# Kernel tuning notes

Hardware: AMD Instinct MI355X
Metric: run time of the kernel (lower is better)

The kernel has to match this reference:

```python
import jax, jax.numpy as jnp
import numpy as np
from jax import lax

B, L, D, DM, S, M, P = 8, 2048, 512, 1024, 32, 4, 4096


def setup_inputs() -> dict:
    key = jax.random.key(0)
    ks = jax.random.split(key, 13)
    emb = jax.random.normal(ks[0], (B, L, D), jnp.float32)
    pos = jax.random.randint(ks[1], (B, L), 1, P + 1)          # pos >= 1 (0 reserved for CLS)
    sid = jax.random.randint(ks[2], (B, L), 0, S)
    mod = jax.random.randint(ks[3], (B, L), 0, M)
    role = jax.random.randint(ks[4], (B, L), 0, 3)
    padding_mask = jax.random.uniform(ks[5], (B, L)) < 0.9
    W_proj = jax.random.normal(ks[6], (S, DM, D), jnp.float32) / np.float32(np.sqrt(D))
    b_proj = jax.random.normal(ks[7], (S, DM), jnp.float32) * 0.01
    cls_content = jax.random.normal(ks[8], (DM,), jnp.float32)
    pos_emb = jax.random.normal(ks[9], (P + 1, DM), jnp.float32) * 0.02
    id_emb = jax.random.normal(ks[10], (S + 1, DM), jnp.float32) * 0.02
    mod_emb = jax.random.normal(ks[11], (M, DM), jnp.float32) * 0.02
    role_emb = jax.random.normal(ks[12], (3, DM), jnp.float32) * 0.02
    return dict(emb=emb, pos=pos, sid=sid, mod=mod, role=role, padding_mask=padding_mask,
                W_proj=W_proj, b_proj=b_proj, cls_content=cls_content,
                pos_emb=pos_emb, id_emb=id_emb, mod_emb=mod_emb, role_emb=role_emb)


def _moe_project(emb, sid, padding_mask, W_proj, b_proj):
    """Per-token per-signal Linear: tokens[b,l] = W_proj[sid[b,l]] @ emb[b,l] + b_proj[sid[b,l]].
    Computed as S dense GEMMs masked per token (dense-dispatch MoE), avoiding an
    O(B*L*DM*D) gathered-weight tensor."""
    def step(acc, sWb):
        s, W, b = sWb
        y = jnp.einsum('bld,od->blo', emb, W) + b  # (B, L, DM)
        m = (sid == s) & padding_mask              # padded tokens stay zero
        return acc + jnp.where(m[..., None], y, 0.0), None
    acc0 = jnp.zeros(emb.shape[:2] + (W_proj.shape[1],), emb.dtype)
    acc, _ = lax.scan(step, acc0, (jnp.arange(W_proj.shape[0]), W_proj, b_proj))
    return acc


def reference(emb, pos, sid, mod, role, padding_mask,
              W_proj, b_proj, cls_content, pos_emb, id_emb, mod_emb, role_emb):
    Bc, Lc = pos.shape
    dm = cls_content.shape[0]
    cls_id = id_emb.shape[0] - 1  # == num_signals

    proj = _moe_project(emb, sid, padding_mask, W_proj, b_proj)  # (B, L, DM)

    cls = jnp.broadcast_to(cls_content, (Bc, 1, dm))
    tokens = jnp.concatenate([cls, proj], axis=1)                # (B, L+1, DM)

    pos_full = jnp.concatenate([jnp.zeros((Bc, 1), pos.dtype), pos], axis=1)
    sid_full = jnp.concatenate([jnp.full((Bc, 1), cls_id, sid.dtype), sid], axis=1)
    tokens = tokens + pos_emb[pos_full] + id_emb[sid_full]

    # modality + role embeddings only on non-CLS tokens (added even where padded, as in torch)
    tokens = tokens.at[:, 1:, :].add(mod_emb[mod] + role_emb[role])

    attn_keep = jnp.concatenate([jnp.ones((Bc, 1), bool), padding_mask], axis=1)
    return tokens, attn_keep
```

## Files before the change

kernel.cpp:

```cpp
#include <hip/hip_runtime.h>
#include <hip/hip_bf16.h>


#define NB   8
#define NL   2048
#define ND   512
#define NDM  1024
#define NS   32
#define NTOK (NB * NL)
#define LP1  (NL + 1)
#define MAXTILES 160
#define EXP_CAP 1024

static __device__ __forceinline__ size_t attn_off() { return (size_t)NB * LP1 * NDM; }

typedef __attribute__((ext_vector_type(8))) short bf16x8;
typedef __attribute__((ext_vector_type(4))) float f32x4;

__device__ __forceinline__ unsigned short f2bf(float f) {
    unsigned int x = __float_as_uint(f);
    x += 0x7fffu + ((x >> 16) & 1u);
    return (unsigned short)(x >> 16);
}

__device__ __forceinline__ float bf2f(unsigned short s) {
    return __uint_as_float(((unsigned int)s) << 16);
}

__device__ __forceinline__ bf16x8 cvt8(float4 a, float4 b) {
    bf16x8 r;
    r[0] = (short)__bfloat16_as_ushort(__float2bfloat16(a.x));
    r[1] = (short)__bfloat16_as_ushort(__float2bfloat16(a.y));
    r[2] = (short)__bfloat16_as_ushort(__float2bfloat16(a.z));
    r[3] = (short)__bfloat16_as_ushort(__float2bfloat16(a.w));
    r[4] = (short)__bfloat16_as_ushort(__float2bfloat16(b.x));
    r[5] = (short)__bfloat16_as_ushort(__float2bfloat16(b.y));
    r[6] = (short)__bfloat16_as_ushort(__float2bfloat16(b.z));
    r[7] = (short)__bfloat16_as_ushort(__float2bfloat16(b.w));
    return r;
}

__device__ __forceinline__ float4 ld4(const float* p) { return *(const float4*)p; }
__device__ __forceinline__ float4 add4(float4 a, float4 b) {
    return make_float4(a.x + b.x, a.y + b.y, a.z + b.z, a.w + b.w);
}

__global__ void k_bucket(const int* __restrict__ sid, const int* __restrict__ mask,
                         const int* __restrict__ mod, const int* __restrict__ role,
                         const float* __restrict__ me, const float* __restrict__ re,
                         int* __restrict__ cnt, int* __restrict__ kidx,
                         int* __restrict__ tokList, float* __restrict__ mrT,
                         float* __restrict__ out) {
    int t = blockIdx.x * 256 + threadIdx.x;
    if (t < NTOK) {
        int s = sid[t];
        bool keep = mask[t] != 0;
        int b = t >> 11, l = t & (NL - 1);
        out[attn_off() + (size_t)b * LP1 + l + 1] = keep ? 1.0f : 0.0f;
        if (t < NB) out[attn_off() + (size_t)t * LP1] = 1.0f;
        int ki = -1;
        if (keep) {
            ki = atomicAdd(&cnt[s], 1);
            if (ki < EXP_CAP) tokList[s * EXP_CAP + ki] = t;
        }
        kidx[t] = ki;
    }
    if (blockIdx.x < 12) {
        int mr = blockIdx.x, m = mr / 3, ro = mr % 3;
        int o = threadIdx.x * 4;
        float4 v = add4(ld4(me + (size_t)m * NDM + o), ld4(re + (size_t)ro * NDM + o));
        *(float4*)&mrT[(size_t)mr * NDM + o] = v;
    }
}

__global__ __launch_bounds__(256) void k_gemm(
    const float* __restrict__ emb, const float* __restrict__ Wp,
    const int* __restrict__ tokList, const int* __restrict__ cnt,
    unsigned short* __restrict__ projC) {
    int e = -1, rowBase = 0, nRows = 0, cBase = 0;
    {
        int T = blockIdx.y, idx = 0, cb = 0;
        for (int s = 0; s < NS; ++s) {
            int c = min(cnt[s], EXP_CAP);
            int nt = (c + 127) >> 7;
            if (T >= idx && T < idx + nt) {
                e = s; rowBase = (T - idx) * 128;
                nRows = min(128, c - rowBase); cBase = cb + rowBase;
            }
            idx += nt; cb += c;
        }
        if (e < 0) return;
    }
    const int nBase = blockIdx.x * 128;

    __shared__ short SA[2][128 * 32];
    __shared__ short SB[2][128 * 32];

    const int tid  = threadIdx.x;
    const int lane = tid & 63;
    const int w    = tid >> 6;
    const int wr   = w >> 1, wc = w & 1;
    const int fr   = lane & 15, kg = lane >> 4;

    const int srow = tid >> 2;
    const int sch  = tid & 3;
    const size_t eBase = (size_t)e * EXP_CAP + rowBase;
    int ar0 = (srow < nRows) ? srow : 0;
    int ar1 = (srow + 64 < nRows) ? srow + 64 : 0;
    int tok0 = tokList[eBase + ar0];
    int tok1 = tokList[eBase + ar1];
    const float* a0 = emb + (size_t)tok0 * ND + sch * 8;
    const float* a1 = emb + (size_t)tok1 * ND + sch * 8;
    const float* b0 = Wp + ((size_t)e * NDM + nBase + srow) * ND + sch * 8;
    const float* b1 = Wp + ((size_t)e * NDM + nBase + srow + 64) * ND + sch * 8;
    const int wo0 = srow * 32 + (sch ^ ((srow >> 1) & 3)) * 8;
    const int wo1 = wo0 + 64 * 32;

    f32x4 acc[4][4];
#pragma unroll
    for (int i = 0; i < 4; ++i)
#pragma unroll
        for (int j = 0; j < 4; ++j)
            acc[i][j] = (f32x4){0.f, 0.f, 0.f, 0.f};

    float4 ta0a, ta0b, ta1a, ta1b, tb0a, tb0b, tb1a, tb1b;
    bf16x8 na0, na1, nb0, nb1;

#define LDF(ks) do {                                           \
        ta0a = ld4(a0 + (ks) * 32); ta0b = ld4(a0 + (ks) * 32 + 4); \
        ta1a = ld4(a1 + (ks) * 32); ta1b = ld4(a1 + (ks) * 32 + 4); \
        tb0a = ld4(b0 + (ks) * 32); tb0b = ld4(b0 + (ks) * 32 + 4); \
        tb1a = ld4(b1 + (ks) * 32); tb1b = ld4(b1 + (ks) * 32 + 4); \
    } while (0)
#define CVT() do {                                             \
        na0 = cvt8(ta0a, ta0b); na1 = cvt8(ta1a, ta1b);        \
        nb0 = cvt8(tb0a, tb0b); nb1 = cvt8(tb1a, tb1b);        \
    } while (0)

    LDF(0); CVT();
    *(bf16x8*)&SA[0][wo0] = na0;
    *(bf16x8*)&SA[0][wo1] = na1;
    *(bf16x8*)&SB[0][wo0] = nb0;
    *(bf16x8*)&SB[0][wo1] = nb1;
    LDF(1); CVT();

    const int pc = kg ^ ((fr >> 1) & 3);
    for (int ks = 0; ks < ND / 32; ++ks) {
        const int cur = ks & 1;
        __syncthreads();
        if (ks < ND / 32 - 1) {
            *(bf16x8*)&SA[cur ^ 1][wo0] = na0;
            *(bf16x8*)&SA[cur ^ 1][wo1] = na1;
            *(bf16x8*)&SB[cur ^ 1][wo0] = nb0;
            *(bf16x8*)&SB[cur ^ 1][wo1] = nb1;
        }
        if (ks < ND / 32 - 2) LDF(ks + 2);
        bf16x8 af[4], bv[4];
#pragma unroll
        for (int i = 0; i < 4; ++i)
            af[i] = *(const bf16x8*)&SA[cur][(wr * 64 + i * 16 + fr) * 32 + pc * 8];
#pragma unroll
        for (int j = 0; j < 4; ++j)
            bv[j] = *(const bf16x8*)&SB[cur][(wc * 64 + j * 16 + fr) * 32 + pc * 8];
#pragma unroll
        for (int i = 0; i < 4; ++i)
#pragma unroll
            for (int j = 0; j < 4; ++j)
                acc[i][j] = __builtin_amdgcn_mfma_f32_16x16x32_bf16(af[i], bv[j], acc[i][j], 0, 0, 0);
        if (ks < ND / 32 - 2) CVT();
    }
#undef LDF
#undef CVT

#pragma unroll
    for (int i = 0; i < 4; ++i) {
#pragma unroll
        for (int r = 0; r < 4; ++r) {
            int row = wr * 64 + i * 16 + kg * 4 + r;
            if (row < nRows) {
                size_t crow = (size_t)(cBase + row) * NDM + nBase;
#pragma unroll
                for (int j = 0; j < 4; ++j)
                    projC[crow + wc * 64 + j * 16 + fr] = f2bf(acc[i][j][r]);
            }
        }
    }
}

__global__ void k_out(const int* __restrict__ pos, const int* __restrict__ sid,
                      const int* __restrict__ mod, const int* __restrict__ role,
                      const int* __restrict__ mask, const int* __restrict__ kidx,
                      const int* __restrict__ cnt,
                      const float* __restrict__ bp, const float* __restrict__ cls_c,
                      const float* __restrict__ pe, const float* __restrict__ ie,
                      const float* __restrict__ mrT,
                      const unsigned short* __restrict__ projC,
                      float* __restrict__ out) {
    __shared__ int scnt[NS];
    if (threadIdx.x < NS) scnt[threadIdx.x] = min(cnt[threadIdx.x], EXP_CAP);
    __syncthreads();
    int rp = threadIdx.x >> 7;
    int o  = (threadIdx.x & 127) * 8;
    int l1 = blockIdx.x * 2 + rp;
    int b  = blockIdx.y;
    if (l1 > NL) return;
    float4 v0, v1;
    if (l1 == 0) {
        const float* ieC = ie + (size_t)NS * NDM;
        v0 = add4(add4(ld4(cls_c + o), ld4(pe + o)), ld4(ieC + o));
        v1 = add4(add4(ld4(cls_c + o + 4), ld4(pe + o + 4)), ld4(ieC + o + 4));
    } else {
        int t = b * NL + l1 - 1;
        int p = pos[t], s = sid[t], mr = mod[t] * 3 + role[t];
        const float* peR = pe + (size_t)p * NDM + o;
        const float* ieR = ie + (size_t)s * NDM + o;
        const float* mrR = mrT + (size_t)mr * NDM + o;
        v0 = add4(add4(ld4(peR), ld4(ieR)), ld4(mrR));
        v1 = add4(add4(ld4(peR + 4), ld4(ieR + 4)), ld4(mrR + 4));
        if (mask[t] != 0) {
            const float* bpR = bp + (size_t)s * NDM + o;
            v0 = add4(v0, ld4(bpR));
            v1 = add4(v1, ld4(bpR + 4));
            int ki = kidx[t];
            if (ki >= 0 && ki < EXP_CAP) {
                int boff = 0;
                for (int q = 0; q < s; ++q) boff += scnt[q];
                const unsigned short* pr = projC + (size_t)(boff + ki) * NDM + o;
                v0.x += bf2f(pr[0]); v0.y += bf2f(pr[1]);
                v0.z += bf2f(pr[2]); v0.w += bf2f(pr[3]);
                v1.x += bf2f(pr[4]); v1.y += bf2f(pr[5]);
                v1.z += bf2f(pr[6]); v1.w += bf2f(pr[7]);
            }
        }
    }
    float* dst = &out[((size_t)b * LP1 + l1) * NDM + o];
    *(float4*)dst = v0;
    *(float4*)(dst + 4) = v1;
}

extern "C" void kernel_launch(void* const* d_in, const int* in_sizes, int n_in,
                              void* d_out, int out_size, void* d_ws, size_t ws_size,
                              hipStream_t stream) {
    const float* emb  = (const float*)d_in[0];
    const int* pos    = (const int*)d_in[1];
    const int* sid    = (const int*)d_in[2];
    const int* mod    = (const int*)d_in[3];
    const int* role   = (const int*)d_in[4];
    const int* mask   = (const int*)d_in[5];
    const float* Wp   = (const float*)d_in[6];
    const float* bp   = (const float*)d_in[7];
    const float* cls  = (const float*)d_in[8];
    const float* pe   = (const float*)d_in[9];
    const float* ie   = (const float*)d_in[10];
    const float* me   = (const float*)d_in[11];
    const float* re   = (const float*)d_in[12];
    float* out = (float*)d_out;

    int* ws        = (int*)d_ws;
    int* cnt       = ws;
    int* tokList   = ws + 1024;
    int* kidx      = ws + 33792;
    float* mrT     = (float*)(ws + 50176);
    unsigned short* projC = (unsigned short*)((char*)d_ws + 262144);

    hipMemsetAsync(cnt, 0, 32 * sizeof(int), stream);
    k_bucket<<<NTOK / 256, 256, 0, stream>>>(sid, mask, mod, role, me, re,
                                             cnt, kidx, tokList, mrT, out);

    dim3 gg(NDM / 128, MAXTILES);
    k_gemm<<<gg, 256, 0, stream>>>(emb, Wp, tokList, cnt, projC);

    dim3 go((LP1 + 1) / 2, NB);
    k_out<<<go, 256, 0, stream>>>(pos, sid, mod, role, mask, kidx, cnt,
                                  bp, cls, pe, ie, mrT, projC, out);
}
```

Measured before the change: 122.6 us.

## Widen GEMM tile to 128x256 with 512 threads to reuse A loads

The grouped-expert GEMM tile grows from 128x128 to 128x256 output columns and the block from 256 to 512 threads (8 waves in a 2x4 grid). Each gathered emb row is now loaded and converted once per 256 output columns instead of once per 128, which halves redundant A traffic and conversion work. The cost is half as many blocks per tile row, so there is less parallelism on a grid that is already sparse in active tiles, along with more shared memory per block and a new launch-bounds occupancy hint.

```diff
diff --git a/kernel.cpp b/kernel.cpp
--- a/kernel.cpp
+++ b/kernel.cpp
@@ -73,7 +73,7 @@
     }
 }
 
-__global__ __launch_bounds__(256) void k_gemm(
+__global__ __launch_bounds__(512, 4) void k_gemm(
     const float* __restrict__ emb, const float* __restrict__ Wp,
     const int* __restrict__ tokList, const int* __restrict__ cnt,
     unsigned short* __restrict__ projC) {
@@ -91,30 +91,30 @@
         }
         if (e < 0) return;
     }
-    const int nBase = blockIdx.x * 128;
+    const int nBase = blockIdx.x * 256;
 
     __shared__ short SA[2][128 * 32];
-    __shared__ short SB[2][128 * 32];
+    __shared__ short SB[2][256 * 32];
 
     const int tid  = threadIdx.x;
     const int lane = tid & 63;
     const int w    = tid >> 6;
-    const int wr   = w >> 1, wc = w & 1;
+    const int wr   = w >> 2, wc = w & 3;
     const int fr   = lane & 15, kg = lane >> 4;
 
-    const int srow = tid >> 2;
-    const int sch  = tid & 3;
+    const int srowA = tid >> 2;
+    const int schA  = tid & 3;
     const size_t eBase = (size_t)e * EXP_CAP + rowBase;
-    int ar0 = (srow < nRows) ? srow : 0;
-    int ar1 = (srow + 64 < nRows) ? srow + 64 : 0;
-    int tok0 = tokList[eBase + ar0];
-    int tok1 = tokList[eBase + ar1];
-    const float* a0 = emb + (size_t)tok0 * ND + sch * 8;
-    const float* a1 = emb + (size_t)tok1 * ND + sch * 8;
-    const float* b0 = Wp + ((size_t)e * NDM + nBase + srow) * ND + sch * 8;
-    const float* b1 = Wp + ((size_t)e * NDM + nBase + srow + 64) * ND + sch * 8;
-    const int wo0 = srow * 32 + (sch ^ ((srow >> 1) & 3)) * 8;
-    const int wo1 = wo0 + 64 * 32;
+    int arA = (srowA < nRows) ? srowA : 0;
+    int tokA = tokList[eBase + arA];
+    const float* aP = emb + (size_t)tokA * ND + schA * 8;
+    const int woA = srowA * 32 + (schA ^ ((srowA >> 1) & 3)) * 8;
+
+    const int srowB = tid >> 1;
+    const int halfB = tid & 1;
+    const float* bP = Wp + ((size_t)e * NDM + nBase + srowB) * ND + halfB * 16;
+    const int woB0 = srowB * 32 + ((halfB * 2)     ^ ((srowB >> 1) & 3)) * 8;
+    const int woB1 = srowB * 32 + ((halfB * 2 + 1) ^ ((srowB >> 1) & 3)) * 8;
 
     f32x4 acc[4][4];
 #pragma unroll
@@ -123,37 +123,32 @@
         for (int j = 0; j < 4; ++j)
             acc[i][j] = (f32x4){0.f, 0.f, 0.f, 0.f};
 
-    float4 ta0a, ta0b, ta1a, ta1b, tb0a, tb0b, tb1a, tb1b;
-    bf16x8 na0, na1, nb0, nb1;
-
-#define LDF(ks) do {                                           \
-        ta0a = ld4(a0 + (ks) * 32); ta0b = ld4(a0 + (ks) * 32 + 4); \
-        ta1a = ld4(a1 + (ks) * 32); ta1b = ld4(a1 + (ks) * 32 + 4); \
-        tb0a = ld4(b0 + (ks) * 32); tb0b = ld4(b0 + (ks) * 32 + 4); \
-        tb1a = ld4(b1 + (ks) * 32); tb1b = ld4(b1 + (ks) * 32 + 4); \
+    float4 ta0, ta1, tb0, tb1, tb2, tb3;
+    bf16x8 na, nb0, nb1;
+
+#define LDF(ks) do {                                            \
+        ta0 = ld4(aP + (ks) * 32); ta1 = ld4(aP + (ks) * 32 + 4); \
+        tb0 = ld4(bP + (ks) * 32); tb1 = ld4(bP + (ks) * 32 + 4); \
+        tb2 = ld4(bP + (ks) * 32 + 8); tb3 = ld4(bP + (ks) * 32 + 12); \
     } while (0)
-#define CVT() do {                                             \
-        na0 = cvt8(ta0a, ta0b); na1 = cvt8(ta1a, ta1b);        \
-        nb0 = cvt8(tb0a, tb0b); nb1 = cvt8(tb1a, tb1b);        \
+#define CVT() do {                                              \
+        na  = cvt8(ta0, ta1);                                   \
+        nb0 = cvt8(tb0, tb1); nb1 = cvt8(tb2, tb3);             \
     } while (0)
-
-    LDF(0); CVT();
-    *(bf16x8*)&SA[0][wo0] = na0;
-    *(bf16x8*)&SA[0][wo1] = na1;
-    *(bf16x8*)&SB[0][wo0] = nb0;
-    *(bf16x8*)&SB[0][wo1] = nb1;
+#define DSW(buf) do {                                           \
+        *(bf16x8*)&SA[buf][woA]  = na;                          \
+        *(bf16x8*)&SB[buf][woB0] = nb0;                         \
+        *(bf16x8*)&SB[buf][woB1] = nb1;                         \
+    } while (0)
+
+    LDF(0); CVT(); DSW(0);
     LDF(1); CVT();
 
     const int pc = kg ^ ((fr >> 1) & 3);
     for (int ks = 0; ks < ND / 32; ++ks) {
         const int cur = ks & 1;
         __syncthreads();
-        if (ks < ND / 32 - 1) {
-            *(bf16x8*)&SA[cur ^ 1][wo0] = na0;
-            *(bf16x8*)&SA[cur ^ 1][wo1] = na1;
-            *(bf16x8*)&SB[cur ^ 1][wo0] = nb0;
-            *(bf16x8*)&SB[cur ^ 1][wo1] = nb1;
-        }
+        if (ks < ND / 32 - 1) DSW(cur ^ 1);
         if (ks < ND / 32 - 2) LDF(ks + 2);
         bf16x8 af[4], bv[4];
 #pragma unroll
@@ -171,6 +166,7 @@
     }
 #undef LDF
 #undef CVT
+#undef DSW
 
 #pragma unroll
     for (int i = 0; i < 4; ++i) {
@@ -267,8 +263,8 @@
     k_bucket<<<NTOK / 256, 256, 0, stream>>>(sid, mask, mod, role, me, re,
                                              cnt, kidx, tokList, mrT, out);
 
-    dim3 gg(NDM / 128, MAXTILES);
-    k_gemm<<<gg, 256, 0, stream>>>(emb, Wp, tokList, cnt, projC);
+    dim3 gg(NDM / 256, MAXTILES);
+    k_gemm<<<gg, 512, 0, stream>>>(emb, Wp, tokList, cnt, projC);
 
     dim3 go((LP1 + 1) / 2, NB);
     k_out<<<go, 256, 0, stream>>>(pos, sid, mod, role, mask, kidx, cnt,
```

Measured after the change: 124.8 us. No clear change (+1.8%).
